# Kernel tuning notes

Measured on AMD Instinct MI355X. Metric: run time of the kernel, lower is better.

Reference implementation:

```python
import jax, jax.numpy as jnp
import numpy as np
from jax import lax

MIN_R = 0.01
RADIUS = 0.8
NSAMPLE = 32
PRED_NSAMPLE = 16
TEMPERATURE = 1.0
DIV_COEF = 10.0
GRID3 = 64  # grid_size**3, grid_size=4
EPS = 1e-5


def _ball_query(q, xyz, radius, nsample):
    """q (M,3), xyz (N,3), radius scalar or (M,). Returns idx (M,nsample) int32, empty (M,) bool.
    Mirrors stack ball_query CUDA op: first-found neighbors within radius, padded with first index."""
    N = xyz.shape[0]
    d2 = jnp.sum((q[:, None, :] - xyz[None, :, :]) ** 2, axis=-1)  # (M,N)
    r = jnp.broadcast_to(jnp.asarray(radius, d2.dtype), (q.shape[0],))[:, None]
    valid = d2 < r * r
    score = jnp.where(valid, -jnp.arange(N, dtype=jnp.int32), -(N + 1))
    vals, _ = lax.top_k(score, nsample)  # largest score == smallest valid index
    idx = -vals
    pad = idx == (N + 1)
    idx = jnp.where(pad, idx[:, :1], idx)  # pad with first found neighbor
    empty = pad[:, 0]                       # no neighbor at all
    idx = jnp.where(empty[:, None], 0, idx)
    return idx, empty


def _group(q, xyz, feats, idx, empty):
    """QueryAndGroup gather: relative xyz concat point features; zero empty queries.
    Returns (M, nsample, 3+C)."""
    g_xyz = xyz[idx] - q[:, None, :]
    g = jnp.concatenate([g_xyz, feats[idx]], axis=-1)
    return jnp.where(empty[:, None, None], jnp.zeros((), g.dtype), g)


def _mlp(x, params):
    """Shared 1x1 Conv2d + BatchNorm2d(training stats) + ReLU stack. x: (B,M,S,C)."""
    for W, g, b in params:
        x = jnp.einsum('bmsc,cd->bmsd', x, W)
        mu = x.mean(axis=(0, 1, 2))
        var = x.var(axis=(0, 1, 2))
        x = (x - mu) * lax.rsqrt(var + EPS) * g + b
        x = jax.nn.relu(x)
    return x


def setup_inputs() -> dict:
    key = jax.random.key(0)
    ks = jax.random.split(key, 16)
    B, N, C, R, Croi = 2, 8192, 32, 64, 128
    scene = jnp.array([10.0, 10.0, 4.0], jnp.float32)
    xyz = jax.random.uniform(ks[0], (B, N, 3), jnp.float32) * scene
    features = jax.random.normal(ks[1], (B, N, C), jnp.float32)
    rois = jax.random.uniform(ks[2], (B, R, GRID3, 3), jnp.float32) * scene
    roi_features = jax.random.normal(ks[3], (B, R, Croi), jnp.float32)

    def kaiming(k, fi, fo):
        return jax.random.normal(k, (fi, fo), jnp.float32) * np.float32(np.sqrt(2.0 / fi))

    return {
        'xyz': xyz, 'features': features, 'rois': rois, 'roi_features': roi_features,
        'temperature_decay': jnp.ones((1,), jnp.float32),
        # predict mlp: [32+3, 32, 32]
        'pw0': kaiming(ks[4], 35, 32), 'pg0': jnp.ones(32), 'pb0': jnp.zeros(32),
        'pw1': kaiming(ks[5], 32, 32), 'pg1': jnp.ones(32), 'pb1': jnp.zeros(32),
        # feat mlp: [32+3, 64, 64]
        'fw0': kaiming(ks[6], 35, 64), 'fg0': jnp.ones(64), 'fb0': jnp.zeros(64),
        'fw1': kaiming(ks[7], 64, 64), 'fg1': jnp.ones(64), 'fb1': jnp.zeros(64),
        # predict fc: [32*64 + 128, 1]
        'fcw': kaiming(ks[8], 2176, 1), 'fcb': jnp.zeros(1),
    }


def reference(xyz, features, rois, roi_features, temperature_decay,
              pw0, pg0, pb0, pw1, pg1, pb1,
              fw0, fg0, fb0, fw1, fg1, fb1, fcw, fcb):
    B, num_rois = rois.shape[0], rois.shape[1]
    new_xyz = rois.reshape(B, -1, 3)  # (B, M, 3), M = num_rois*grid^3

    # ---- radius-prediction branch: fixed-radius grouping + MLP + max-pool ----
    idx_p, empty_p = jax.vmap(lambda q, x: _ball_query(q, x, RADIUS, PRED_NSAMPLE))(new_xyz, xyz)
    gp = jax.vmap(_group)(new_xyz, xyz, features, idx_p, empty_p)  # (B,M,S,3+C)
    gp = _mlp(gp, [(pw0, pg0, pb0), (pw1, pg1, pb1)])
    pooled = gp.max(axis=2)                       # (B, M, Cp)
    pooled = pooled.reshape(B, num_rois, -1)      # (B, R, grid^3*Cp)
    res = jnp.concatenate([pooled, roi_features], axis=-1) @ fcw + fcb  # (B,R,1)
    r = jnp.maximum(res / DIV_COEF + RADIUS, MIN_R)
    r_pts = jnp.broadcast_to(r, (B, num_rois, GRID3)).reshape(B, -1)    # (B, M)

    # ---- deformable branch: per-query radius grouping + soft weights ----
    idx_d, empty_d = jax.vmap(lambda q, x, rr: _ball_query(q, x, rr, NSAMPLE))(new_xyz, xyz, r_pts)
    gd = jax.vmap(_group)(new_xyz, xyz, features, idx_d, empty_d)       # (B,M,S,3+C)
    dist = jnp.linalg.norm(gd[..., :3], axis=-1)                        # (B,M,S)
    w = jax.nn.sigmoid((r_pts[..., None] - dist) / (TEMPERATURE * temperature_decay[0]))
    w = jnp.where(empty_d[..., None], jnp.zeros((), w.dtype), w)
    gd = _mlp(gd, [(fw0, fg0, fb0), (fw1, fg1, fb1)])                   # (B,M,S,Cout)
    new_feats = (w[..., None] * gd).max(axis=2)                          # (B,M,Cout)

    return new_xyz.reshape(-1, 3), new_feats.reshape(-1, new_feats.shape[-1])
```

## Files before the change

### kernel.cpp

```cpp
#include <hip/hip_runtime.h>
#include <hip/hip_fp16.h>

#define NB 2
#define NPTS 8192
#define NQ 4096
#define MTOT 8192
#define SP 16
#define SD 32
#define CIN 32
#define CP 32
#define CF 64
#define NROI 128
#define RADIUS_C 0.8f
#define MIN_R_C 0.01f
#define DIV_COEF_C 10.0f

#define INV_CS 1.25f
#define NCX 13
#define NCY 13
#define NCZ 5
#define NCELL (NCX * NCY * NCZ)

__device__ int    g_idx_p[MTOT * SP];
__device__ int    g_empty_p[MTOT];
__device__ int    g_idx_d[MTOT * SD];
__device__ int    g_empty_d[MTOT];
__device__ int    g_cellcnt[NB][NCELL];
__device__ int    g_cellcur[NB][NCELL];
__device__ int    g_cellstart[NB][NCELL + 1];
__device__ float4 g_cellxyzw[NB][NPTS];
__device__ unsigned char g_xa[(size_t)MTOT * SD * CF * 2];
__device__ unsigned char g_xb[(size_t)MTOT * SD * CF * 2];
__device__ unsigned int g_w1h[CF * CF / 2];
__device__ unsigned int g_w0h[CF * 32];
__device__ float  g_psT[CF * 2048];
__device__ float  g_pqT[CF * 2048];
__device__ float  g_bnscale[4][CF];
__device__ float  g_bnshift[4][CF];
__device__ float  g_rroi[NROI];

typedef _Float16 h2v  __attribute__((ext_vector_type(2)));
typedef _Float16 f16x8 __attribute__((ext_vector_type(8)));
typedef float    f32x4 __attribute__((ext_vector_type(4)));

__device__ __forceinline__ int cell_of(float x, float y, float z) {
    int cx = min(NCX - 1, max(0, (int)floorf(x * INV_CS)));
    int cy = min(NCY - 1, max(0, (int)floorf(y * INV_CS)));
    int cz = min(NCZ - 1, max(0, (int)floorf(z * INV_CS)));
    return (cz * NCY + cy) * NCX + cx;
}

#define SETUP_N (MTOT * 3 + CF * CF / 2 + CF * 32 + NB * NCELL)
__global__ void setup_kernel(const float* __restrict__ rois, const float* __restrict__ fw1,
                             const float* __restrict__ fw0, float* __restrict__ out) {
    int i = blockIdx.x * 256 + threadIdx.x;
    if (i < MTOT * 3) { out[i] = rois[i]; return; }
    i -= MTOT * 3;
    if (i < CF * CF / 2) {
        int ch = i >> 5, c2 = i & 31;
        __half2 h = __floats2half2_rn(fw1[(2 * c2) * CF + ch], fw1[(2 * c2 + 1) * CF + ch]);
        g_w1h[i] = *(unsigned int*)&h;
        return;
    }
    i -= CF * CF / 2;
    if (i < CF * 32) {
        int ch = i >> 5, c2 = i & 31;
        float a = (2 * c2     < 35) ? fw0[(2 * c2) * CF + ch]     : 0.f;
        float b = (2 * c2 + 1 < 35) ? fw0[(2 * c2 + 1) * CF + ch] : 0.f;
        __half2 h = __floats2half2_rn(a, b);
        g_w0h[i] = *(unsigned int*)&h;
        return;
    }
    i -= CF * 32;
    if (i < NB * NCELL) ((int*)g_cellcnt)[i] = 0;
}

__global__ void grid_count_kernel(const float* __restrict__ xyz) {
    int i = blockIdx.x * 256 + threadIdx.x;
    int b = i >> 13;
    int cell = cell_of(xyz[(size_t)i * 3 + 0], xyz[(size_t)i * 3 + 1], xyz[(size_t)i * 3 + 2]);
    atomicAdd(&g_cellcnt[b][cell], 1);
}

__global__ void grid_prefix_kernel() {
    __shared__ int sc[1024];
    int b = blockIdx.x, tid = threadIdx.x;
    int v = (tid < NCELL) ? g_cellcnt[b][tid] : 0;
    sc[tid] = v;
    __syncthreads();
    for (int off = 1; off < 1024; off <<= 1) {
        int add = (tid >= off) ? sc[tid - off] : 0;
        __syncthreads();
        sc[tid] += add;
        __syncthreads();
    }
    if (tid < NCELL) {
        int excl = sc[tid] - v;
        g_cellstart[b][tid] = excl;
        g_cellcur[b][tid] = excl;
    }
    if (tid == 0) g_cellstart[b][NCELL] = NPTS;
}

__global__ void grid_scatter_kernel(const float* __restrict__ xyz) {
    int i = blockIdx.x * 256 + threadIdx.x;
    int b = i >> 13, il = i & (NPTS - 1);
    float x = xyz[(size_t)i * 3 + 0];
    float y = xyz[(size_t)i * 3 + 1];
    float z = xyz[(size_t)i * 3 + 2];
    int cell = cell_of(x, y, z);
    int pos = atomicAdd(&g_cellcur[b][cell], 1);
    g_cellxyzw[b][pos] = make_float4(x, y, z, __int_as_float(il));
}

template <int NS>
__launch_bounds__(256, 8)
__global__ void bq_grid_kernel(const float* __restrict__ xyz, const float* __restrict__ newxyz) {
    __shared__ int s_cand[4][512];
    __shared__ int s_meta[4][2];
    int tid = threadIdx.x, wv = tid >> 6, lane = tid & 63;
    int q = blockIdx.x * 4 + wv;
    int b = q >> 12;
    float qx = newxyz[q * 3 + 0], qy = newxyz[q * 3 + 1], qz = newxyz[q * 3 + 2];
    float r = (NS == SP) ? RADIUS_C : g_rroi[q >> 6];
    float r2 = r * r;
    int* idx_out   = (NS == SP) ? g_idx_p   : g_idx_d;
    int* empty_out = (NS == SP) ? g_empty_p : g_empty_d;

    if (lane == 0) s_meta[wv][0] = 0;
    __asm__ volatile("s_waitcnt lgkmcnt(0)" ::: "memory");

    float rp = r + 1e-4f;
    int xlo = max(0, min(NCX - 1, (int)floorf((qx - rp) * INV_CS)));
    int xhi = max(0, min(NCX - 1, (int)floorf((qx + rp) * INV_CS)));
    int ylo = max(0, min(NCY - 1, (int)floorf((qy - rp) * INV_CS)));
    int yhi = max(0, min(NCY - 1, (int)floorf((qy + rp) * INV_CS)));
    int zlo = max(0, min(NCZ - 1, (int)floorf((qz - rp) * INV_CS)));
    int zhi = max(0, min(NCZ - 1, (int)floorf((qz + rp) * INV_CS)));
    int nx = xhi - xlo + 1, ny = yhi - ylo + 1, nz = zhi - zlo + 1;
    int ncell = nx * ny * nz;

    bool ovf = false;
    for (int ci = lane; ci < ncell; ci += 64) {
        int cx = xlo + (ci % nx);
        int t1 = ci / nx;
        int cy = ylo + (t1 % ny);
        int cz = zlo + (t1 / ny);
        int cell = (cz * NCY + cy) * NCX + cx;
        int s0 = g_cellstart[b][cell], e0 = g_cellstart[b][cell + 1];
        for (int e = s0; e < e0; ++e) {
            float4 v = g_cellxyzw[b][e];
            float dx = qx - v.x, dy = qy - v.y, dz = qz - v.z;
            if (dx * dx + dy * dy + dz * dz < r2) {
                int pos = atomicAdd(&s_meta[wv][0], 1);
                if (pos < 512) s_cand[wv][pos] = __float_as_int(v.w);
                else ovf = true;
            }
        }
    }
    __asm__ volatile("s_waitcnt lgkmcnt(0) vmcnt(0)" ::: "memory");
    int cnt = s_meta[wv][0];

    if (__ballot(ovf)) {
        const float* xb = xyz + (size_t)b * NPTS * 3;
        int cnt2 = 0, first_idx = 0;
        for (int g = 0; g < NPTS / 64 && cnt2 < NS; ++g) {
            int p = (g << 6) + lane;
            float dx = qx - xb[3 * p + 0];
            float dy = qy - xb[3 * p + 1];
            float dz = qz - xb[3 * p + 2];
            bool valid = (dx * dx + dy * dy + dz * dz) < r2;
            unsigned long long mask = __ballot(valid);
            if (cnt2 == 0 && mask) first_idx = (g << 6) + (int)__builtin_ctzll(mask);
            int pos = cnt2 + __popcll(mask & ((1ull << lane) - 1ull));
            if (valid && pos < NS) idx_out[q * NS + pos] = p;
            cnt2 += (int)__popcll(mask);
        }
        if (cnt2 == 0) {
            if (lane < NS) idx_out[q * NS + lane] = 0;
            if (lane == 0) empty_out[q] = 1;
        } else {
            int filled = cnt2 < NS ? cnt2 : NS;
            if (lane >= filled && lane < NS) idx_out[q * NS + lane] = first_idx;
            if (lane == 0) empty_out[q] = 0;
        }
        return;
    }

    if (cnt == 0) {
        if (lane < NS) idx_out[q * NS + lane] = 0;
        if (lane == 0) empty_out[q] = 1;
        return;
    }
    for (int i = lane; i < cnt; i += 64) {
        int c = s_cand[wv][i];
        int rank = 0;
        for (int j = 0; j < cnt; ++j) rank += (s_cand[wv][j] < c) ? 1 : 0;
        if (rank < NS) idx_out[q * NS + rank] = c;
        if (rank == 0) s_meta[wv][1] = c;
    }
    __asm__ volatile("s_waitcnt lgkmcnt(0)" ::: "memory");
    if (cnt < NS && lane >= cnt && lane < NS) idx_out[q * NS + lane] = s_meta[wv][1];
    if (lane == 0) empty_out[q] = 0;
}

template <int NS, int CH, bool HALF>
__launch_bounds__(256, 6)
__global__ void mlp_passA_kernel(const float* __restrict__ xyz, const float* __restrict__ feats,
                                 const float* __restrict__ newxyz, const float* __restrict__ W0,
                                 void* __restrict__ xout_) {
    constexpr int GSTR = 37;
    constexpr int SST  = CH + 2;
    constexpr int CHH  = CH / 2;
    __shared__ float buf[128 * GSTR];
    __shared__ float ls[256], lq[256];
    int tid = threadIdx.x;
    int row = tid & 127, half = tid >> 7;
    int halfu = __builtin_amdgcn_readfirstlane(half);
    int rowbase = blockIdx.x * 128;
    int grow = rowbase + row;
    int q = grow / NS, b = q >> 12;
    const int* idx_arr = (NS == SP) ? g_idx_p : g_idx_d;
    const int* emp_arr = (NS == SP) ? g_empty_p : g_empty_d;
    {
        float* dst = &buf[row * GSTR];
        if (emp_arr[q]) {
            int c0 = half ? 18 : 0, c1 = half ? 35 : 18;
            for (int c = c0; c < c1; ++c) dst[c] = 0.f;
        } else {
            int idx = idx_arr[grow];
            if (half == 0) {
                const float* xp = xyz + (size_t)b * NPTS * 3 + idx * 3;
                dst[0] = xp[0] - newxyz[q * 3 + 0];
                dst[1] = xp[1] - newxyz[q * 3 + 1];
                dst[2] = xp[2] - newxyz[q * 3 + 2];
            }
            const float4* fp = (const float4*)(feats + (size_t)b * NPTS * CIN + (size_t)idx * CIN);
#pragma unroll
            for (int j = 0; j < 4; ++j) {
                float4 v = fp[half * 4 + j];
                float* d = dst + 3 + (half * 4 + j) * 4;
                d[0] = v.x; d[1] = v.y; d[2] = v.z; d[3] = v.w;
            }
        }
    }
    __syncthreads();
    float acc[CHH];
#pragma unroll
    for (int ch = 0; ch < CHH; ++ch) acc[ch] = 0.f;
    {
        const float* inrow = &buf[row * GSTR];
        const float* w = W0 + halfu * CHH;
        for (int c = 0; c < 35; ++c) {
            float h = inrow[c];
#pragma unroll
            for (int ch = 0; ch < CHH; ++ch) acc[ch] = fmaf(h, w[c * CH + ch], acc[ch]);
        }
    }
    float* xf = (float*)xout_;
    __half* xh = (__half*)xout_;
    float sum = 0.f, sq = 0.f;
#pragma unroll
    for (int p = 0; p < 2; ++p) {
        __syncthreads();
        if ((row >> 6) == p) {
            float* srow = &buf[(row & 63) * SST + half * CHH];
#pragma unroll
            for (int ch = 0; ch < CHH; ++ch) srow[ch] = acc[ch];
        }
        __syncthreads();
        if (CH == 64) {
            int ch = tid & 63, rg = tid >> 6;
            for (int r = 0; r < 16; ++r) {
                float v = buf[(rg * 16 + r) * SST + ch];
                size_t o = (size_t)(rowbase + p * 64 + rg * 16 + r) * CH + ch;
                if (HALF) xh[o] = __float2half_rn(v); else xf[o] = v;
                sum += v; sq += v * v;
            }
        } else {
            int ch = tid & 31, rg = tid >> 5;
            for (int r = 0; r < 8; ++r) {
                float v = buf[(rg * 8 + r) * SST + ch];
                size_t o = (size_t)(rowbase + p * 64 + rg * 8 + r) * CH + ch;
                if (HALF) xh[o] = __float2half_rn(v); else xf[o] = v;
                sum += v; sq += v * v;
            }
        }
    }
    ls[tid] = sum; lq[tid] = sq;
    __syncthreads();
    if (CH == 64) {
        if (tid < 64) {
            g_psT[tid * 2048 + blockIdx.x] = ls[tid] + ls[64 + tid] + ls[128 + tid] + ls[192 + tid];
            g_pqT[tid * 2048 + blockIdx.x] = lq[tid] + lq[64 + tid] + lq[128 + tid] + lq[192 + tid];
        }
    } else {
        if (tid < 32) {
            float s = 0.f, qq = 0.f;
#pragma unroll
            for (int k = 0; k < 8; ++k) { s += ls[tid + 32 * k]; qq += lq[tid + 32 * k]; }
            g_psT[tid * 2048 + blockIdx.x] = s;
            g_pqT[tid * 2048 + blockIdx.x] = qq;
        }
    }
}

__launch_bounds__(256, 4)
__global__ void mlp_fA_kernel(const float* __restrict__ xyz, const float* __restrict__ feats,
                              const float* __restrict__ newxyz, __half* __restrict__ xout) {
    __shared__ __align__(16) unsigned int hp[128 * 36];
    __shared__ float lsum[4][64], lsq[4][64];
    int tid = threadIdx.x, wv = tid >> 6, lane = tid & 63;
    int rowbase = blockIdx.x * 128;
    {
        int row = tid >> 1, part = tid & 1;
        int grow = rowbase + row;
        int q = grow / SD, b = q >> 12;
        unsigned int* d = &hp[row * 36 + part * 9];
        if (g_empty_d[q]) {
#pragma unroll
            for (int p = 0; p < 9; ++p) d[p] = 0u;
        } else {
            int idx = g_idx_d[grow];
            const float4* fp = (const float4*)(feats + (size_t)b * NPTS * CIN + (size_t)idx * CIN);
            float kv[18];
            if (part == 0) {
                const float* xp = xyz + (size_t)b * NPTS * 3 + idx * 3;
                kv[0] = xp[0] - newxyz[q * 3 + 0];
                kv[1] = xp[1] - newxyz[q * 3 + 1];
                kv[2] = xp[2] - newxyz[q * 3 + 2];
                float4 v0 = fp[0], v1 = fp[1], v2 = fp[2], v3 = fp[3];
                kv[3] = v0.x; kv[4] = v0.y; kv[5] = v0.z; kv[6] = v0.w;
                kv[7] = v1.x; kv[8] = v1.y; kv[9] = v1.z; kv[10] = v1.w;
                kv[11] = v2.x; kv[12] = v2.y; kv[13] = v2.z; kv[14] = v2.w;
                kv[15] = v3.x; kv[16] = v3.y; kv[17] = v3.z;
            } else {
                float4 v3 = fp[3], v4 = fp[4], v5 = fp[5], v6 = fp[6], v7 = fp[7];
                kv[0] = v3.w;
                kv[1] = v4.x; kv[2] = v4.y; kv[3] = v4.z; kv[4] = v4.w;
                kv[5] = v5.x; kv[6] = v5.y; kv[7] = v5.z; kv[8] = v5.w;
                kv[9] = v6.x; kv[10] = v6.y; kv[11] = v6.z; kv[12] = v6.w;
                kv[13] = v7.x; kv[14] = v7.y; kv[15] = v7.z; kv[16] = v7.w;
                kv[17] = 0.f;
            }
#pragma unroll
            for (int p = 0; p < 9; ++p) {
                __half2 hh = __floats2half2_rn(kv[2 * p], kv[2 * p + 1]);
                d[p] = *(unsigned int*)&hh;
            }
        }
        unsigned int* z = &hp[row * 36 + 18 + part * 7];
#pragma unroll
        for (int p = 0; p < 7; ++p) z[p] = 0u;
    }
    f16x8 bf[4][2];
    {
        int chl = lane & 15, kg = lane >> 4;
#pragma unroll
        for (int ct = 0; ct < 4; ++ct)
#pragma unroll
            for (int kt = 0; kt < 2; ++kt)
                bf[ct][kt] = *(const f16x8*)(g_w0h + (ct * 16 + chl) * 32 + kt * 16 + kg * 4);
    }
    __syncthreads();
    f32x4 acc[2][4];
#pragma unroll
    for (int rt = 0; rt < 2; ++rt)
#pragma unroll
        for (int ct = 0; ct < 4; ++ct) acc[rt][ct] = (f32x4){0.f, 0.f, 0.f, 0.f};
#pragma unroll
    for (int rt = 0; rt < 2; ++rt) {
        int row = wv * 32 + rt * 16 + (lane & 15);
#pragma unroll
        for (int kt = 0; kt < 2; ++kt) {
            f16x8 a = *(const f16x8*)&hp[row * 36 + kt * 16 + (lane >> 4) * 4];
#pragma unroll
            for (int ct = 0; ct < 4; ++ct)
                acc[rt][ct] = __builtin_amdgcn_mfma_f32_16x16x32_f16(a, bf[ct][kt], acc[rt][ct], 0, 0, 0);
        }
    }
    float s[4] = {0.f, 0.f, 0.f, 0.f}, q[4] = {0.f, 0.f, 0.f, 0.f};
#pragma unroll
    for (int rt = 0; rt < 2; ++rt) {
        int rbase = rowbase + wv * 32 + rt * 16 + (lane >> 4) * 4;
#pragma unroll
        for (int ct = 0; ct < 4; ++ct) {
            int ch = ct * 16 + (lane & 15);
#pragma unroll
            for (int i = 0; i < 4; ++i) {
                float v = acc[rt][ct][i];
                xout[(size_t)(rbase + i) * CF + ch] = __float2half_rn(v);
                s[ct] += v; q[ct] += v * v;
            }
        }
    }
#pragma unroll
    for (int ct = 0; ct < 4; ++ct) {
        s[ct] += __shfl_xor(s[ct], 16, 64); s[ct] += __shfl_xor(s[ct], 32, 64);
        q[ct] += __shfl_xor(q[ct], 16, 64); q[ct] += __shfl_xor(q[ct], 32, 64);
    }
    if (lane < 16) {
#pragma unroll
        for (int ct = 0; ct < 4; ++ct) {
            lsum[wv][ct * 16 + lane] = s[ct];
            lsq[wv][ct * 16 + lane] = q[ct];
        }
    }
    __syncthreads();
    if (tid < 64) {
        g_psT[tid * 2048 + blockIdx.x] = lsum[0][tid] + lsum[1][tid] + lsum[2][tid] + lsum[3][tid];
        g_pqT[tid * 2048 + blockIdx.x] = lsq[0][tid] + lsq[1][tid] + lsq[2][tid] + lsq[3][tid];
    }
}

template <int NS, int CH>
__launch_bounds__(128, 4)
__global__ void mlp_passB_kernel(const float* __restrict__ W1, const float* __restrict__ xin,
                                 float* __restrict__ xout, int bn0) {
    constexpr int HSTR = 33;
    constexpr int SST  = CH + 2;
    __shared__ float buf[128 * 37];
    __shared__ float ls[128], lq[128];
    int tid = threadIdx.x;
    int rowbase = blockIdx.x * 128;
    const float* sc0 = g_bnscale[bn0];
    const float* sh0 = g_bnshift[bn0];
    float acc2[CH];
#pragma unroll
    for (int ch = 0; ch < CH; ++ch) acc2[ch] = 0.f;
    const float4* src = (const float4*)xin;
#pragma unroll
    for (int hc = 0; hc < CH / 32; ++hc) {
        if (hc) __syncthreads();
#pragma unroll
        for (int k = 0; k < 8; ++k) {
            int o4 = tid + k * 128;
            int rloc = o4 >> 3, j = o4 & 7;
            int c = 4 * j, gc = hc * 32 + c;
            float4 v = src[(size_t)(rowbase + rloc) * (CH / 4) + hc * 8 + j];
            float* d = &buf[rloc * HSTR + c];
            d[0] = fmaxf(fmaf(v.x, sc0[gc + 0], sh0[gc + 0]), 0.f);
            d[1] = fmaxf(fmaf(v.y, sc0[gc + 1], sh0[gc + 1]), 0.f);
            d[2] = fmaxf(fmaf(v.z, sc0[gc + 2], sh0[gc + 2]), 0.f);
            d[3] = fmaxf(fmaf(v.w, sc0[gc + 3], sh0[gc + 3]), 0.f);
        }
        __syncthreads();
        const float* hrow = &buf[tid * HSTR];
        for (int c = 0; c < 32; ++c) {
            float h = hrow[c];
#pragma unroll
            for (int ch = 0; ch < CH; ++ch)
                acc2[ch] = fmaf(h, W1[(hc * 32 + c) * CH + ch], acc2[ch]);
        }
    }
    float sum = 0.f, sq = 0.f;
#pragma unroll
    for (int p = 0; p < 2; ++p) {
        __syncthreads();
        if ((tid >> 6) == p) {
            float* srow = &buf[(tid & 63) * SST];
#pragma unroll
            for (int ch = 0; ch < CH; ++ch) srow[ch] = acc2[ch];
        }
        __syncthreads();
        int ch = tid & 31, rg = tid >> 5;
        for (int r = 0; r < 16; ++r) {
            float v = buf[(rg * 16 + r) * SST + ch];
            xout[(size_t)(rowbase + p * 64 + rg * 16 + r) * CH + ch] = v;
            sum += v; sq += v * v;
        }
    }
    ls[tid] = sum; lq[tid] = sq;
    __syncthreads();
    if (tid < 32) {
        g_psT[tid * 2048 + blockIdx.x] = ls[tid] + ls[32 + tid] + ls[64 + tid] + ls[96 + tid];
        g_pqT[tid * 2048 + blockIdx.x] = lq[tid] + lq[32 + tid] + lq[64 + tid] + lq[96 + tid];
    }
}

__launch_bounds__(256, 4)
__global__ void mlp_fB_kernel(const __half* __restrict__ xin, __half* __restrict__ xout) {
    __shared__ __align__(16) unsigned int hp[128 * 36];
    __shared__ float lsum[4][64], lsq[4][64];
    int tid = threadIdx.x, wv = tid >> 6, lane = tid & 63;
    int rowbase = blockIdx.x * 128;
    const float* sc0 = g_bnscale[2];
    const float* sh0 = g_bnshift[2];
    {
        const float4* src = (const float4*)xin;
#pragma unroll
        for (int k = 0; k < 4; ++k) {
            int o4 = tid + k * 256;
            int rloc = o4 >> 3, j = o4 & 7;
            float4 v = src[(size_t)(rowbase + rloc) * 8 + j];
            const __half2* ph = (const __half2*)&v;
            unsigned int* d = &hp[rloc * 36 + 4 * j];
#pragma unroll
            for (int m = 0; m < 4; ++m) {
                float2 f = __half22float2(ph[m]);
                int gc = 8 * j + 2 * m;
                float a = fmaxf(fmaf(f.x, sc0[gc + 0], sh0[gc + 0]), 0.f);
                float bb = fmaxf(fmaf(f.y, sc0[gc + 1], sh0[gc + 1]), 0.f);
                __half2 hh = __floats2half2_rn(a, bb);
                d[m] = *(unsigned int*)&hh;
            }
        }
    }
    f16x8 bf[4][2];
    {
        int chl = lane & 15, kg = lane >> 4;
#pragma unroll
        for (int ct = 0; ct < 4; ++ct)
#pragma unroll
            for (int kt = 0; kt < 2; ++kt)
                bf[ct][kt] = *(const f16x8*)(g_w1h + (ct * 16 + chl) * 32 + kt * 16 + kg * 4);
    }
    __syncthreads();
    f32x4 acc[2][4];
#pragma unroll
    for (int rt = 0; rt < 2; ++rt)
#pragma unroll
        for (int ct = 0; ct < 4; ++ct) acc[rt][ct] = (f32x4){0.f, 0.f, 0.f, 0.f};
#pragma unroll
    for (int rt = 0; rt < 2; ++rt) {
        int row = wv * 32 + rt * 16 + (lane & 15);
#pragma unroll
        for (int kt = 0; kt < 2; ++kt) {
            f16x8 a = *(const f16x8*)&hp[row * 36 + kt * 16 + (lane >> 4) * 4];
#pragma unroll
            for (int ct = 0; ct < 4; ++ct)
                acc[rt][ct] = __builtin_amdgcn_mfma_f32_16x16x32_f16(a, bf[ct][kt], acc[rt][ct], 0, 0, 0);
        }
    }
    float s[4] = {0.f, 0.f, 0.f, 0.f}, q[4] = {0.f, 0.f, 0.f, 0.f};
#pragma unroll
    for (int rt = 0; rt < 2; ++rt) {
        int rbase = rowbase + wv * 32 + rt * 16 + (lane >> 4) * 4;
#pragma unroll
        for (int ct = 0; ct < 4; ++ct) {
            int ch = ct * 16 + (lane & 15);
#pragma unroll
            for (int i = 0; i < 4; ++i) {
                float v = acc[rt][ct][i];
                xout[(size_t)(rbase + i) * CF + ch] = __float2half_rn(v);
                s[ct] += v; q[ct] += v * v;
            }
        }
    }
#pragma unroll
    for (int ct = 0; ct < 4; ++ct) {
        s[ct] += __shfl_xor(s[ct], 16, 64); s[ct] += __shfl_xor(s[ct], 32, 64);
        q[ct] += __shfl_xor(q[ct], 16, 64); q[ct] += __shfl_xor(q[ct], 32, 64);
    }
    if (lane < 16) {
#pragma unroll
        for (int ct = 0; ct < 4; ++ct) {
            lsum[wv][ct * 16 + lane] = s[ct];
            lsq[wv][ct * 16 + lane] = q[ct];
        }
    }
    __syncthreads();
    if (tid < 64) {
        g_psT[tid * 2048 + blockIdx.x] = lsum[0][tid] + lsum[1][tid] + lsum[2][tid] + lsum[3][tid];
        g_pqT[tid * 2048 + blockIdx.x] = lsq[0][tid] + lsq[1][tid] + lsq[2][tid] + lsq[3][tid];
    }
}

__global__ void finalize_kernel(const float* __restrict__ gamma, const float* __restrict__ beta,
                                float n, int layer, int nblocks) {
    __shared__ double l_s[256], l_q[256];
    int ch = blockIdx.x, tid = threadIdx.x;
    double s = 0, q = 0;
    for (int i = tid; i < nblocks; i += 256) { s += g_psT[ch * 2048 + i]; q += g_pqT[ch * 2048 + i]; }
    l_s[tid] = s; l_q[tid] = q; __syncthreads();
    for (int off = 128; off > 0; off >>= 1) {
        if (tid < off) { l_s[tid] += l_s[tid + off]; l_q[tid] += l_q[tid + off]; }
        __syncthreads();
    }
    if (tid == 0) {
        double mu = l_s[0] / (double)n;
        double var = l_q[0] / (double)n - mu * mu;
        if (var < 0) var = 0;
        double sc = (double)gamma[ch] / sqrt(var + 1e-5);
        g_bnscale[layer][ch] = (float)sc;
        g_bnshift[layer][ch] = (float)((double)beta[ch] - mu * sc);
    }
}

__global__ void passC_f_kernel(const float* __restrict__ xyz, const float* __restrict__ newxyz,
                               const float* __restrict__ td, const __half* __restrict__ xin,
                               float* __restrict__ out) {
    __shared__ float lw[64];
    int tid = threadIdx.x;
    int qpair = blockIdx.x * 2;
    if (tid < 64) {
        int ql = tid >> 5, s = tid & 31;
        int q = qpair + ql;
        float wv = 0.f;
        if (!g_empty_d[q]) {
            int idx = g_idx_d[q * SD + s];
            int b = q >> 12;
            float dx = xyz[(size_t)b * NPTS * 3 + idx * 3 + 0] - newxyz[q * 3 + 0];
            float dy = xyz[(size_t)b * NPTS * 3 + idx * 3 + 1] - newxyz[q * 3 + 1];
            float dz = xyz[(size_t)b * NPTS * 3 + idx * 3 + 2] - newxyz[q * 3 + 2];
            float dist = sqrtf(dx * dx + dy * dy + dz * dz);
            float rq = g_rroi[q >> 6];
            wv = 1.f / (1.f + expf(-(rq - dist) / td[0]));
        }
        lw[tid] = wv;
    }
    __syncthreads();
    int ql = tid >> 6, ch = tid & 63;
    int q = qpair + ql;
    float sc = g_bnscale[3][ch], sh = g_bnshift[3][ch];
    float m = 0.f;
    for (int s = 0; s < SD; ++s) {
        float v = __half2float(xin[((size_t)q * SD + s) * CF + ch]);
        m = fmaxf(m, lw[ql * 32 + s] * fmaxf(fmaf(v, sc, sh), 0.f));
    }
    out[MTOT * 3 + (size_t)q * CF + ch] = m;
}

__global__ void passC_roi_kernel(const float* __restrict__ fcw, const float* __restrict__ fcb,
                                 const float* __restrict__ roif, const float* __restrict__ xin) {
    __shared__ float red[256];
    int tid = threadIdx.x;
    int roi = blockIdx.x;
    int ch = tid & 31, qs = tid >> 5;
    float sc = g_bnscale[1][ch], sh = g_bnshift[1][ch];
    float acc = 0.f;
    for (int ql = qs; ql < 64; ql += 8) {
        int q = roi * 64 + ql;
        float m = 0.f;
        for (int s = 0; s < SP; ++s) {
            float v = xin[(size_t)(q * SP + s) * CP + ch] * sc + sh;
            m = fmaxf(m, fmaxf(v, 0.f));
        }
        acc += m * fcw[ql * CP + ch];
    }
    if (tid < 128) acc += roif[roi * 128 + tid] * fcw[2048 + tid];
    red[tid] = acc;
    __syncthreads();
    for (int off = 128; off > 0; off >>= 1) {
        if (tid < off) red[tid] += red[tid + off];
        __syncthreads();
    }
    if (tid == 0)
        g_rroi[roi] = fmaxf((red[0] + fcb[0]) / DIV_COEF_C + RADIUS_C, MIN_R_C);
}

extern "C" void kernel_launch(void* const* d_in, const int* in_sizes, int n_in,
                              void* d_out, int out_size, void* d_ws, size_t ws_size,
                              hipStream_t stream) {
    const float* xyz   = (const float*)d_in[0];
    const float* feats = (const float*)d_in[1];
    const float* rois  = (const float*)d_in[2];
    const float* roif  = (const float*)d_in[3];
    const float* td    = (const float*)d_in[4];
    const float* pw0 = (const float*)d_in[5];
    const float* pg0 = (const float*)d_in[6];
    const float* pb0 = (const float*)d_in[7];
    const float* pw1 = (const float*)d_in[8];
    const float* pg1 = (const float*)d_in[9];
    const float* pb1 = (const float*)d_in[10];
    const float* fw0 = (const float*)d_in[11];
    const float* fg0 = (const float*)d_in[12];
    const float* fb0 = (const float*)d_in[13];
    const float* fw1 = (const float*)d_in[14];
    const float* fg1 = (const float*)d_in[15];
    const float* fb1 = (const float*)d_in[16];
    const float* fcw = (const float*)d_in[17];
    const float* fcb = (const float*)d_in[18];
    float* out = (float*)d_out;

    void* xa; hipGetSymbolAddress(&xa, HIP_SYMBOL(g_xa));
    void* xb; hipGetSymbolAddress(&xb, HIP_SYMBOL(g_xb));

    setup_kernel<<<(SETUP_N + 255) / 256, 256, 0, stream>>>(rois, fw1, fw0, out);
    grid_count_kernel<<<64, 256, 0, stream>>>(xyz);
    grid_prefix_kernel<<<2, 1024, 0, stream>>>();
    grid_scatter_kernel<<<64, 256, 0, stream>>>(xyz);

    bq_grid_kernel<SP><<<MTOT / 4, 256, 0, stream>>>(xyz, rois);
    mlp_passA_kernel<SP, CP, false><<<1024, 256, 0, stream>>>(xyz, feats, rois, pw0, xa);
    finalize_kernel<<<CP, 256, 0, stream>>>(pg0, pb0, (float)(MTOT * SP), 0, 1024);
    mlp_passB_kernel<SP, CP><<<1024, 128, 0, stream>>>(pw1, (const float*)xa, (float*)xb, 0);
    finalize_kernel<<<CP, 256, 0, stream>>>(pg1, pb1, (float)(MTOT * SP), 1, 1024);
    passC_roi_kernel<<<NROI, 256, 0, stream>>>(fcw, fcb, roif, (const float*)xb);

    bq_grid_kernel<SD><<<MTOT / 4, 256, 0, stream>>>(xyz, rois);
    mlp_fA_kernel<<<2048, 256, 0, stream>>>(xyz, feats, rois, (__half*)xa);
    finalize_kernel<<<CF, 256, 0, stream>>>(fg0, fb0, (float)(MTOT * SD), 2, 2048);
    mlp_fB_kernel<<<2048, 256, 0, stream>>>((const __half*)xa, (__half*)xb);
    finalize_kernel<<<CF, 256, 0, stream>>>(fg1, fb1, (float)(MTOT * SD), 3, 2048);
    passC_f_kernel<<<MTOT / 2, 128, 0, stream>>>(xyz, rois, td, (const __half*)xb, out);
}
```

Baseline: 255.5 us.

## Fuse grid build and setup into one prep kernel with shared-memory counting

Merges the setup, grid count, prefix scan and scatter kernels into a single prep_kernel. Two 1024-thread blocks each build the spatial grid for one batch using shared-memory atomics, and the remaining blocks do the roi copy and fp16 weight packing. This removes three kernel launches and the global atomics. It also raises the occupancy hint on the two fp16 MLP kernels from 4 to 5 blocks, which may constrain registers. The scatter order within a cell stays nondeterministic, as it was before.

```diff
diff --git a/kernel.cpp b/kernel.cpp
--- a/kernel.cpp
+++ b/kernel.cpp
@@ -25,8 +25,6 @@
 __device__ int    g_empty_p[MTOT];
 __device__ int    g_idx_d[MTOT * SD];
 __device__ int    g_empty_d[MTOT];
-__device__ int    g_cellcnt[NB][NCELL];
-__device__ int    g_cellcur[NB][NCELL];
 __device__ int    g_cellstart[NB][NCELL + 1];
 __device__ float4 g_cellxyzw[NB][NPTS];
 __device__ unsigned char g_xa[(size_t)MTOT * SD * CF * 2];
@@ -50,67 +48,72 @@
     return (cz * NCY + cy) * NCX + cx;
 }
 
-#define SETUP_N (MTOT * 3 + CF * CF / 2 + CF * 32 + NB * NCELL)
-__global__ void setup_kernel(const float* __restrict__ rois, const float* __restrict__ fw1,
-                             const float* __restrict__ fw0, float* __restrict__ out) {
-    int i = blockIdx.x * 256 + threadIdx.x;
-    if (i < MTOT * 3) { out[i] = rois[i]; return; }
-    i -= MTOT * 3;
-    if (i < CF * CF / 2) {
+#define COPY_N  (MTOT * 3)
+#define PACK1_N (CF * CF / 2)
+#define PACK0_N (CF * 32)
+__launch_bounds__(1024)
+__global__ void prep_kernel(const float* __restrict__ xyz, const float* __restrict__ rois,
+                            const float* __restrict__ fw1, const float* __restrict__ fw0,
+                            float* __restrict__ out) {
+    int blk = blockIdx.x, tid = threadIdx.x;
+    if (blk < 2) {
+        __shared__ int sc[1024];
+        __shared__ int lcur[NCELL];
+        int b = blk;
+        if (tid < NCELL) lcur[tid] = 0;
+        __syncthreads();
+        float px[8], py[8], pz[8]; int pc[8];
+        const float* xb = xyz + (size_t)b * NPTS * 3;
+#pragma unroll
+        for (int k = 0; k < 8; ++k) {
+            int p = tid + k * 1024;
+            float x = xb[3 * p + 0], y = xb[3 * p + 1], z = xb[3 * p + 2];
+            px[k] = x; py[k] = y; pz[k] = z;
+            int c = cell_of(x, y, z);
+            pc[k] = c;
+            atomicAdd(&lcur[c], 1);
+        }
+        __syncthreads();
+        int v = (tid < NCELL) ? lcur[tid] : 0;
+        sc[tid] = v;
+        __syncthreads();
+        for (int off = 1; off < 1024; off <<= 1) {
+            int add = (tid >= off) ? sc[tid - off] : 0;
+            __syncthreads();
+            sc[tid] += add;
+            __syncthreads();
+        }
+        if (tid < NCELL) {
+            int excl = sc[tid] - v;
+            g_cellstart[b][tid] = excl;
+            lcur[tid] = excl;
+        }
+        if (tid == 0) g_cellstart[b][NCELL] = NPTS;
+        __syncthreads();
+#pragma unroll
+        for (int k = 0; k < 8; ++k) {
+            int pos = atomicAdd(&lcur[pc[k]], 1);
+            g_cellxyzw[b][pos] = make_float4(px[k], py[k], pz[k], __int_as_float(tid + k * 1024));
+        }
+        return;
+    }
+    int i = (blk - 2) * 1024 + tid;
+    if (i < COPY_N) { out[i] = rois[i]; return; }
+    i -= COPY_N;
+    if (i < PACK1_N) {
         int ch = i >> 5, c2 = i & 31;
         __half2 h = __floats2half2_rn(fw1[(2 * c2) * CF + ch], fw1[(2 * c2 + 1) * CF + ch]);
         g_w1h[i] = *(unsigned int*)&h;
         return;
     }
-    i -= CF * CF / 2;
-    if (i < CF * 32) {
+    i -= PACK1_N;
+    if (i < PACK0_N) {
         int ch = i >> 5, c2 = i & 31;
         float a = (2 * c2     < 35) ? fw0[(2 * c2) * CF + ch]     : 0.f;
-        float b = (2 * c2 + 1 < 35) ? fw0[(2 * c2 + 1) * CF + ch] : 0.f;
-        __half2 h = __floats2half2_rn(a, b);
+        float b2 = (2 * c2 + 1 < 35) ? fw0[(2 * c2 + 1) * CF + ch] : 0.f;
+        __half2 h = __floats2half2_rn(a, b2);
         g_w0h[i] = *(unsigned int*)&h;
-        return;
-    }
-    i -= CF * 32;
-    if (i < NB * NCELL) ((int*)g_cellcnt)[i] = 0;
-}
-
-__global__ void grid_count_kernel(const float* __restrict__ xyz) {
-    int i = blockIdx.x * 256 + threadIdx.x;
-    int b = i >> 13;
-    int cell = cell_of(xyz[(size_t)i * 3 + 0], xyz[(size_t)i * 3 + 1], xyz[(size_t)i * 3 + 2]);
-    atomicAdd(&g_cellcnt[b][cell], 1);
-}
-
-__global__ void grid_prefix_kernel() {
-    __shared__ int sc[1024];
-    int b = blockIdx.x, tid = threadIdx.x;
-    int v = (tid < NCELL) ? g_cellcnt[b][tid] : 0;
-    sc[tid] = v;
-    __syncthreads();
-    for (int off = 1; off < 1024; off <<= 1) {
-        int add = (tid >= off) ? sc[tid - off] : 0;
-        __syncthreads();
-        sc[tid] += add;
-        __syncthreads();
-    }
-    if (tid < NCELL) {
-        int excl = sc[tid] - v;
-        g_cellstart[b][tid] = excl;
-        g_cellcur[b][tid] = excl;
-    }
-    if (tid == 0) g_cellstart[b][NCELL] = NPTS;
-}
-
-__global__ void grid_scatter_kernel(const float* __restrict__ xyz) {
-    int i = blockIdx.x * 256 + threadIdx.x;
-    int b = i >> 13, il = i & (NPTS - 1);
-    float x = xyz[(size_t)i * 3 + 0];
-    float y = xyz[(size_t)i * 3 + 1];
-    float z = xyz[(size_t)i * 3 + 2];
-    int cell = cell_of(x, y, z);
-    int pos = atomicAdd(&g_cellcur[b][cell], 1);
-    g_cellxyzw[b][pos] = make_float4(x, y, z, __int_as_float(il));
+    }
 }
 
 template <int NS>
@@ -305,7 +308,7 @@
     }
 }
 
-__launch_bounds__(256, 4)
+__launch_bounds__(256, 5)
 __global__ void mlp_fA_kernel(const float* __restrict__ xyz, const float* __restrict__ feats,
                               const float* __restrict__ newxyz, __half* __restrict__ xout) {
     __shared__ __align__(16) unsigned int hp[128 * 36];
@@ -478,7 +481,7 @@
     }
 }
 
-__launch_bounds__(256, 4)
+__launch_bounds__(256, 5)
 __global__ void mlp_fB_kernel(const __half* __restrict__ xin, __half* __restrict__ xout) {
     __shared__ __align__(16) unsigned int hp[128 * 36];
     __shared__ float lsum[4][64], lsq[4][64];
@@ -676,10 +679,7 @@
     void* xa; hipGetSymbolAddress(&xa, HIP_SYMBOL(g_xa));
     void* xb; hipGetSymbolAddress(&xb, HIP_SYMBOL(g_xb));
 
-    setup_kernel<<<(SETUP_N + 255) / 256, 256, 0, stream>>>(rois, fw1, fw0, out);
-    grid_count_kernel<<<64, 256, 0, stream>>>(xyz);
-    grid_prefix_kernel<<<2, 1024, 0, stream>>>();
-    grid_scatter_kernel<<<64, 256, 0, stream>>>(xyz);
+    prep_kernel<<<30, 1024, 0, stream>>>(xyz, rois, fw1, fw0, out);
 
     bq_grid_kernel<SP><<<MTOT / 4, 256, 0, stream>>>(xyz, rois);
     mlp_passA_kernel<SP, CP, false><<<1024, 256, 0, stream>>>(xyz, feats, rois, pw0, xa);
```

Result: no change. 258.6 us (+1.2%).
